# Kernel optimization log

Measured on AMD Instinct MI355X. Metric: run time of the kernel, lower is better.

The kernel has to match this reference:

```python
import jax, jax.numpy as jnp
import numpy as np

WINDOW = 1024
HOP = 256

def setup_inputs() -> dict:
    key = jax.random.key(0)
    X = jax.random.normal(key, (16, 2, 262144), dtype=jnp.float32)
    return {"X": X}

def reference(X):
    # X: (B, 2, T) with channel 0 = Re, channel 1 = Im.
    # Identity-weight Conv1d(1, window, kernel=window, stride=hop) is exactly
    # strided framing: frame t is X[..., t*hop : t*hop + window].
    B, _, T = X.shape
    n_frames = (T - WINDOW) // HOP + 1
    # (n_frames, WINDOW) gather index into the time axis
    idx = jnp.arange(n_frames)[:, None] * HOP + jnp.arange(WINDOW)[None, :]
    frames = X[:, :, idx]                      # (B, 2, n_frames, WINDOW)
    return jnp.transpose(frames, (0, 1, 3, 2)) # (B, 2, WINDOW, n_frames)
```

## Files before the change

### kernel.cpp

```cpp
#include <hip/hip_runtime.h>

#define WINDOW_SZ 1024
#define HOP_SZ    256
#define NFRAMES   1021
#define T_LEN     262144

#define NLINES 1024
#define WG_ROWS 16

typedef float f4  __attribute__((ext_vector_type(4)));
typedef float f4u __attribute__((ext_vector_type(4), aligned(4)));

__global__ __launch_bounds__(512)
void frame_transpose_kernel(const float* __restrict__ X,
                            float* __restrict__ out) {
    __shared__ float lds[WG_ROWS * NLINES];

    const int bid = blockIdx.x;
    const int bc  = bid >> 4;
    const int wg  = bid & 15;
    const int t   = threadIdx.x;

    const float* Xbc = X + (size_t)bc * T_LEN + wg * 16;

#pragma unroll
    for (int p = 0; p < 8; ++p) {
        const int idx  = p * 512 + t;
        const int line = idx >> 2;
        const int sub  = idx & 3;
        const f4 v = *(const f4*)(Xbc + line * HOP_SZ + 4 * sub);
        lds[(4 * sub + 0) * NLINES + line] = v.x;
        lds[(4 * sub + 1) * NLINES + line] = v.y;
        lds[(4 * sub + 2) * NLINES + line] = v.z;
        lds[(4 * sub + 3) * NLINES + line] = v.w;
    }

    __syncthreads();

#pragma unroll
    for (int k = 0; k < 4; ++k) {
        float* obase = out + (size_t)(bc * WINDOW_SZ + 256 * k + 16 * wg) * NFRAMES;
#pragma unroll
        for (int p = 0; p < 8; ++p) {
            const int slot = p * 512 + t;
            const int row  = slot >> 8;
            const int pos  = slot & 255;
            const float* lrow = &lds[row * NLINES + 4 * pos];
            if (pos < 255) {
                const f4 q0 = *(const f4*)(lrow);
                const f4 q1 = *(const f4*)(lrow + 4);
                f4 o;
                if      (k == 0) o = q0;
                else if (k == 1) o = f4{q0.y, q0.z, q0.w, q1.x};
                else if (k == 2) o = f4{q0.z, q0.w, q1.x, q1.y};
                else             o = f4{q0.w, q1.x, q1.y, q1.z};
                *(f4u*)(obase + (size_t)row * NFRAMES + 4 * pos) = o;
            } else {
                obase[(size_t)row * NFRAMES + 1020] = lrow[k];
            }
        }
    }
}

extern "C" void kernel_launch(void* const* d_in, const int* in_sizes, int n_in,
                              void* d_out, int out_size, void* d_ws, size_t ws_size,
                              hipStream_t stream) {
    const float* X = (const float*)d_in[0];
    float* out = (float*)d_out;

    dim3 block(512, 1, 1);
    dim3 grid(32 * 16, 1, 1);
    frame_transpose_kernel<<<grid, block, 0, stream>>>(X, out);
}
```

Measured before the change: 157.4 us.

## Split frame axis into four chunks per workgroup with smaller LDS tiles

Each workgroup now handles a 256-frame chunk of one 16-row window slab instead of all 1021 frames. The grid grows fourfold, with 256-thread blocks and about 16 KB of LDS each instead of 64 KB. This should allow more resident workgroups per CU and better latency hiding on this memory-bound framing and transpose. In exchange, four overlapping lines per chunk are loaded twice, and the index math and boundary checks become more complex.

```diff
diff --git a/kernel.cpp b/kernel.cpp
--- a/kernel.cpp
+++ b/kernel.cpp
@@ -4,60 +4,70 @@
 #define HOP_SZ    256
 #define NFRAMES   1021
 #define T_LEN     262144
+#define NLINES_TOT 1024
 
-#define NLINES 1024
-#define WG_ROWS 16
+#define CHUNK  256
+#define SLINES 260
+#define LSTR   260
 
 typedef float f4  __attribute__((ext_vector_type(4)));
 typedef float f4u __attribute__((ext_vector_type(4), aligned(4)));
 
-__global__ __launch_bounds__(512)
+__global__ __launch_bounds__(256, 8)
 void frame_transpose_kernel(const float* __restrict__ X,
                             float* __restrict__ out) {
-    __shared__ float lds[WG_ROWS * NLINES];
+    __shared__ float lds[16 * LSTR];
 
     const int bid = blockIdx.x;
-    const int bc  = bid >> 4;
-    const int wg  = bid & 15;
+    const int fc  = bid & 3;
+    const int wg  = (bid >> 2) & 15;
+    const int bc  = bid >> 6;
     const int t   = threadIdx.x;
 
-    const float* Xbc = X + (size_t)bc * T_LEN + wg * 16;
+    const int L0 = fc * CHUNK;
+    const float* Xb = X + (size_t)bc * T_LEN + wg * 16;
 
 #pragma unroll
-    for (int p = 0; p < 8; ++p) {
-        const int idx  = p * 512 + t;
-        const int line = idx >> 2;
-        const int sub  = idx & 3;
-        const f4 v = *(const f4*)(Xbc + line * HOP_SZ + 4 * sub);
-        lds[(4 * sub + 0) * NLINES + line] = v.x;
-        lds[(4 * sub + 1) * NLINES + line] = v.y;
-        lds[(4 * sub + 2) * NLINES + line] = v.z;
-        lds[(4 * sub + 3) * NLINES + line] = v.w;
+    for (int p = 0; p < 5; ++p) {
+        const int idx = p * 256 + t;
+        if (idx < 4 * SLINES) {
+            const int line = idx >> 2;
+            const int sub  = idx & 3;
+            if (L0 + line < NLINES_TOT) {
+                const f4 v = *(const f4*)(Xb + (size_t)(L0 + line) * HOP_SZ + 4 * sub);
+                const int r0 = 4 * sub;
+                lds[(r0 + 0) * LSTR + line] = v.x;
+                lds[(r0 + 1) * LSTR + line] = v.y;
+                lds[(r0 + 2) * LSTR + line] = v.z;
+                lds[(r0 + 3) * LSTR + line] = v.w;
+            }
+        }
     }
 
     __syncthreads();
 
+    float* outb = out + ((size_t)(bc * WINDOW_SZ + 16 * wg)) * NFRAMES + fc * CHUNK;
 #pragma unroll
-    for (int k = 0; k < 4; ++k) {
-        float* obase = out + (size_t)(bc * WINDOW_SZ + 256 * k + 16 * wg) * NFRAMES;
-#pragma unroll
-        for (int p = 0; p < 8; ++p) {
-            const int slot = p * 512 + t;
-            const int row  = slot >> 8;
-            const int pos  = slot & 255;
-            const float* lrow = &lds[row * NLINES + 4 * pos];
-            if (pos < 255) {
-                const f4 q0 = *(const f4*)(lrow);
-                const f4 q1 = *(const f4*)(lrow + 4);
-                f4 o;
-                if      (k == 0) o = q0;
-                else if (k == 1) o = f4{q0.y, q0.z, q0.w, q1.x};
-                else if (k == 2) o = f4{q0.z, q0.w, q1.x, q1.y};
-                else             o = f4{q0.w, q1.x, q1.y, q1.z};
-                *(f4u*)(obase + (size_t)row * NFRAMES + 4 * pos) = o;
-            } else {
-                obase[(size_t)row * NFRAMES + 1020] = lrow[k];
-            }
+    for (int p = 0; p < 16; ++p) {
+        const int slot = p * 256 + t;
+        const int k    = slot >> 10;
+        const int rem  = slot & 1023;
+        const int row  = rem >> 6;
+        const int pos  = rem & 63;
+        const int fbase = L0 + 4 * pos;
+        const float* lrow = &lds[row * LSTR + 4 * pos];
+        float* oaddr = outb + (size_t)(256 * k + row) * NFRAMES + 4 * pos;
+        if (fbase + 3 <= NFRAMES - 1) {
+            const f4 q0 = *(const f4*)(lrow);
+            const f4 q1 = *(const f4*)(lrow + 4);
+            f4 o;
+            if      (k == 0) o = q0;
+            else if (k == 1) o = f4{q0.y, q0.z, q0.w, q1.x};
+            else if (k == 2) o = f4{q0.z, q0.w, q1.x, q1.y};
+            else             o = f4{q0.w, q1.x, q1.y, q1.z};
+            *(f4u*)oaddr = o;
+        } else if (fbase <= NFRAMES - 1) {
+            *oaddr = lrow[k];
         }
     }
 }
@@ -68,7 +78,7 @@
     const float* X = (const float*)d_in[0];
     float* out = (float*)d_out;
 
-    dim3 block(512, 1, 1);
-    dim3 grid(32 * 16, 1, 1);
+    dim3 block(256, 1, 1);
+    dim3 grid(32 * 16 * 4, 1, 1);
     frame_transpose_kernel<<<grid, block, 0, stream>>>(X, out);
 }
```

New measurement: 162.8 us. +3.4%, slower.

## Software-pipeline frame transpose over four line chunks with double-buffered LDS

Applied to the files above, without the earlier changes.

Splits each workgroup's 1024 input lines into four chunks of 256 (plus a 4-line halo) and double-buffers them in LDS. The global load of the next chunk is issued into registers before the current chunk is transposed and stored, so memory latency overlaps with work. LDS use drops from 64KB to about 33KB, which may allow more resident workgroups. The cost is extra barriers, more halo rereads, predicated edge handling, and a few more registers.

```diff
diff --git a/kernel.cpp b/kernel.cpp
--- a/kernel.cpp
+++ b/kernel.cpp
@@ -4,9 +4,13 @@
 #define HOP_SZ    256
 #define NFRAMES   1021
 #define T_LEN     262144
+#define NLINES_TOT 1024
 
-#define NLINES 1024
-#define WG_ROWS 16
+#define CHUNK   256
+#define NCHUNK  4
+#define SL      260
+#define LSTR    260
+#define TASKS   (SL * 4)
 
 typedef float f4  __attribute__((ext_vector_type(4)));
 typedef float f4u __attribute__((ext_vector_type(4), aligned(4)));
@@ -14,39 +18,55 @@
 __global__ __launch_bounds__(512)
 void frame_transpose_kernel(const float* __restrict__ X,
                             float* __restrict__ out) {
-    __shared__ float lds[WG_ROWS * NLINES];
+    __shared__ float lds[2][16 * LSTR];
 
     const int bid = blockIdx.x;
     const int bc  = bid >> 4;
     const int wg  = bid & 15;
     const int t   = threadIdx.x;
 
-    const float* Xbc = X + (size_t)bc * T_LEN + wg * 16;
+    const float* Xb   = X   + (size_t)bc * T_LEN + wg * 16;
+    float*       outb = out + (size_t)(bc * WINDOW_SZ + 16 * wg) * NFRAMES;
 
+    auto stage_load = [&](int c, f4* v) {
 #pragma unroll
-    for (int p = 0; p < 8; ++p) {
-        const int idx  = p * 512 + t;
-        const int line = idx >> 2;
-        const int sub  = idx & 3;
-        const f4 v = *(const f4*)(Xbc + line * HOP_SZ + 4 * sub);
-        lds[(4 * sub + 0) * NLINES + line] = v.x;
-        lds[(4 * sub + 1) * NLINES + line] = v.y;
-        lds[(4 * sub + 2) * NLINES + line] = v.z;
-        lds[(4 * sub + 3) * NLINES + line] = v.w;
-    }
-
-    __syncthreads();
-
+        for (int p = 0; p < 3; ++p) {
+            const int idx  = p * 512 + t;
+            const int line = idx >> 2;
+            const int sub  = idx & 3;
+            const int gl   = c * CHUNK + line;
+            v[p] = f4{0.f, 0.f, 0.f, 0.f};
+            if (idx < TASKS && gl < NLINES_TOT)
+                v[p] = *(const f4*)(Xb + (size_t)gl * HOP_SZ + 4 * sub);
+        }
+    };
+    auto stage_write = [&](float* buf, const f4* v) {
 #pragma unroll
-    for (int k = 0; k < 4; ++k) {
-        float* obase = out + (size_t)(bc * WINDOW_SZ + 256 * k + 16 * wg) * NFRAMES;
+        for (int p = 0; p < 3; ++p) {
+            const int idx  = p * 512 + t;
+            const int line = idx >> 2;
+            const int sub  = idx & 3;
+            if (idx < TASKS) {
+                const int r0 = 4 * sub;
+                buf[(r0 + 0) * LSTR + line] = v[p].x;
+                buf[(r0 + 1) * LSTR + line] = v[p].y;
+                buf[(r0 + 2) * LSTR + line] = v[p].z;
+                buf[(r0 + 3) * LSTR + line] = v[p].w;
+            }
+        }
+    };
+    auto compute = [&](const float* buf, int c) {
 #pragma unroll
-        for (int p = 0; p < 8; ++p) {
-            const int slot = p * 512 + t;
-            const int row  = slot >> 8;
-            const int pos  = slot & 255;
-            const float* lrow = &lds[row * NLINES + 4 * pos];
-            if (pos < 255) {
+        for (int q = 0; q < 8; ++q) {
+            const int slot = q * 512 + t;
+            const int k    = slot >> 10;
+            const int rem  = slot & 1023;
+            const int row  = rem >> 6;
+            const int pos  = rem & 63;
+            const int fb   = c * CHUNK + 4 * pos;
+            const float* lrow = buf + row * LSTR + 4 * pos;
+            float* oaddr = outb + (size_t)(256 * k + row) * NFRAMES + fb;
+            if (fb + 3 < NFRAMES) {
                 const f4 q0 = *(const f4*)(lrow);
                 const f4 q1 = *(const f4*)(lrow + 4);
                 f4 o;
@@ -54,12 +74,38 @@
                 else if (k == 1) o = f4{q0.y, q0.z, q0.w, q1.x};
                 else if (k == 2) o = f4{q0.z, q0.w, q1.x, q1.y};
                 else             o = f4{q0.w, q1.x, q1.y, q1.z};
-                *(f4u*)(obase + (size_t)row * NFRAMES + 4 * pos) = o;
-            } else {
-                obase[(size_t)row * NFRAMES + 1020] = lrow[k];
+                *(f4u*)oaddr = o;
+            } else if (fb < NFRAMES) {
+                *oaddr = lrow[k];
             }
         }
-    }
+    };
+
+    f4 vA[3], vB[3];
+
+    stage_load(0, vA);
+    stage_write(lds[0], vA);
+    __syncthreads();
+
+    stage_load(1, vB);
+    compute(lds[0], 0);
+    __syncthreads();
+    stage_write(lds[1], vB);
+    __syncthreads();
+
+    stage_load(2, vA);
+    compute(lds[1], 1);
+    __syncthreads();
+    stage_write(lds[0], vA);
+    __syncthreads();
+
+    stage_load(3, vB);
+    compute(lds[0], 2);
+    __syncthreads();
+    stage_write(lds[1], vB);
+    __syncthreads();
+
+    compute(lds[1], 3);
 }
 
 extern "C" void kernel_launch(void* const* d_in, const int* in_sizes, int n_in,
```

New measurement: 163.1 us. 1.04x slower.
